# Kernel optimization log

Measured on AMD Instinct MI355X. Metric: run time of the kernel, lower is better.

Reference implementation:

```python
import jax, jax.numpy as jnp
import numpy as np

DIM = 768
H = 12
HD = 64  # head_dim = dim // num_heads
SCALE = HD ** (-0.5)
EPS = 1e-6


def setup_inputs() -> dict:
    key = jax.random.key(0)
    k1, k2, k3, k4, k5 = jax.random.split(key, 5)
    B, N = 8, 1024
    x = jax.random.normal(k1, (B, N, DIM), dtype=jnp.float32)
    policy = jax.random.uniform(k2, (B, N, 1), dtype=jnp.float32)
    # nn.Linear weights: [out_features, in_features]; qkv_bias=False, proj has bias
    qkv_w = jax.random.normal(k3, (3 * H * HD, DIM), dtype=jnp.float32) * (DIM ** -0.5)
    proj_w = jax.random.normal(k4, (DIM, H * HD), dtype=jnp.float32) * ((H * HD) ** -0.5)
    proj_b = jax.random.normal(k5, (DIM,), dtype=jnp.float32) * 0.01
    return {"x": x, "policy": policy, "qkv_w": qkv_w, "proj_w": proj_w, "proj_b": proj_b}


def _softmax_with_policy(attn, policy):
    # attn: [B,H,N,N], policy: [B,N,1]
    B, Hh, N, _ = attn.shape
    attn_policy = policy.reshape(B, 1, 1, N)
    eye = jnp.eye(N, dtype=attn_policy.dtype).reshape(1, 1, N, N)
    attn_policy = attn_policy + (1.0 - attn_policy) * eye
    max_att = jnp.max(attn, axis=-1, keepdims=True)
    a = jnp.exp((attn - max_att).astype(jnp.float32)) * attn_policy.astype(jnp.float32)
    a = (a + EPS / N) / (jnp.sum(a, axis=-1, keepdims=True) + EPS)
    return a.astype(max_att.dtype)


def reference(x, policy, qkv_w, proj_w, proj_b):
    B, N, C = x.shape
    qkv = (x @ qkv_w.T).reshape(B, N, 3, H, HD)
    qkv = jnp.transpose(qkv, (2, 0, 3, 1, 4))  # [3,B,H,N,HD]
    q, k, v = qkv[0], qkv[1], qkv[2]
    attn = jnp.einsum('bhnd,bhmd->bhnm', q * SCALE, k)  # [B,H,N,N]
    attn = _softmax_with_policy(attn, policy)
    out = jnp.einsum('bhnm,bhmd->bhnd', attn, v)  # [B,H,N,HD]
    out = jnp.transpose(out, (0, 2, 1, 3)).reshape(B, N, H * HD)
    return out @ proj_w.T + proj_b
```

## Files before the change

kernel.cpp:

```cpp
#include <hip/hip_runtime.h>

typedef __bf16 bf16x8 __attribute__((ext_vector_type(8)));
typedef float floatx4 __attribute__((ext_vector_type(4)));

#define EPSF 1e-6f

__device__ inline unsigned short f2bf(float f) {
  union { float f; unsigned u; } x; x.f = f;
  unsigned r = x.u + 0x7FFFu + ((x.u >> 16) & 1u);
  return (unsigned short)(r >> 16);
}
__device__ inline float bf2f(unsigned short u) {
  union { unsigned u; float f; } x; x.u = ((unsigned)u) << 16;
  return x.f;
}
__device__ inline unsigned pk2bf(float lo, float hi) {
  union { float f; unsigned u; } a, b; a.f = lo; b.f = hi;
  unsigned ua = a.u + 0x8000u, ub = b.u + 0x8000u;
  return (ub & 0xFFFF0000u) | (ua >> 16);
}
__device__ inline unsigned cvtpk(float lo, float hi) {
  unsigned r;
  asm("v_cvt_pk_bf16_f32 %0, %1, %2" : "=v"(r) : "v"(lo), "v"(hi));
  return r;
}
__device__ inline float fexp2(float x) { return __builtin_amdgcn_exp2f(x); }

__device__ inline floatx4 mfma16(bf16x8 a, bf16x8 b, floatx4 c) {
  return __builtin_amdgcn_mfma_f32_16x16x32_bf16(a, b, c, 0, 0, 0);
}

__device__ inline void gll16(const unsigned short* g, unsigned short* l) {
  __builtin_amdgcn_global_load_lds((__attribute__((address_space(1))) void*)g,
                                   (__attribute__((address_space(3))) void*)l, 16, 0, 0);
}

__device__ __host__ inline int sigma_inv(int p) {
  const int qq = p >> 3, jj = p & 7;
  return (jj < 4) ? (qq * 4 + jj) : (16 + qq * 4 + jj - 4);
}

__global__ __launch_bounds__(256) void prep_kernel(const float* __restrict__ x,
                                                   const float* __restrict__ qkv_w,
                                                   const float* __restrict__ proj_w,
                                                   const float* __restrict__ policy,
                                                   unsigned short* __restrict__ xb,
                                                   unsigned short* __restrict__ wqkv,
                                                   unsigned short* __restrict__ wproj,
                                                   unsigned short* __restrict__ pbf) {
  const int bid = blockIdx.x, tid = threadIdx.x;
  if (bid < 3072) {
    const int i = bid * 2048 + tid * 8;
    float4 v0 = *(const float4*)(x + i);
    float4 v1 = *(const float4*)(x + i + 4);
    __align__(16) unsigned short o[8] = {f2bf(v0.x), f2bf(v0.y), f2bf(v0.z), f2bf(v0.w),
                                         f2bf(v1.x), f2bf(v1.y), f2bf(v1.z), f2bf(v1.w)};
    *(float4*)(xb + i) = *(float4*)o;
  } else if (bid < 3936) {
    const int i = (bid - 3072) * 2048 + tid * 8;
    const float s = (i < 589824) ? 0.18033688011112042f : 1.0f;
    float4 v0 = *(const float4*)(qkv_w + i);
    float4 v1 = *(const float4*)(qkv_w + i + 4);
    __align__(16) unsigned short o[8] = {
        f2bf(v0.x * s), f2bf(v0.y * s), f2bf(v0.z * s), f2bf(v0.w * s),
        f2bf(v1.x * s), f2bf(v1.y * s), f2bf(v1.z * s), f2bf(v1.w * s)};
    *(float4*)(wqkv + i) = *(float4*)o;
  } else if (bid < 4224) {
    const int i0 = (bid - 3936) * 2048 + tid * 8;
    const int base = (i0 / 768) * 768 + ((i0 % 768) & ~63);
    __align__(16) unsigned short o[8];
#pragma unroll
    for (int t = 0; t < 8; t++) {
      const int cp = (i0 + t) & 63;
      const int c = 16 * (cp & 3) + (cp >> 2);
      o[t] = f2bf(proj_w[base + c]);
    }
    *(float4*)(wproj + i0) = *(float4*)o;
  } else {
    const int idx = (bid - 4224) * 256 + tid;
    const int b = idx >> 10, g = idx & 1023;
    const int c = ((g >> 5) << 5) + sigma_inv(g & 31);
    pbf[idx] = f2bf(policy[b * 1024 + c]);
  }
}

template <int EP, int BN, int W>
__global__ __launch_bounds__(256, W) void gemm_bt(const unsigned short* __restrict__ A,
                                                  const unsigned short* __restrict__ Bt,
                                                  void* __restrict__ Cout,
                                                  const float* __restrict__ bias,
                                                  int M, int N, int K) {
  constexpr int J = BN / 32;
  __shared__ __align__(16) unsigned short sA[128 * 64];
  __shared__ __align__(16) unsigned short sB[BN * 64];
  const int bid = blockIdx.x;
  const int yb = (bid & 7) * 8 + ((bid >> 3) & 7);
  const int xb_ = bid >> 6;
  const int m0 = yb * 128, n0 = xb_ * BN;
  const int tid = threadIdx.x;
  const int lane = tid & 63, wave = tid >> 6;
  const int qd = lane >> 4, l15 = lane & 15;
  const int wr = (wave >> 1) * 64, wc = (wave & 1) * (BN / 2);
  const int srow = tid >> 3;
  const int scb = (tid & 7) ^ (srow & 7);
  const unsigned short* Ag = A + (long)(m0 + srow) * K + scb * 8;
  const unsigned short* Bg = Bt + (long)(n0 + srow) * K + scb * 8;
  const int x7 = l15 & 7;
  floatx4 acc[4][J] = {};
  for (int k0 = 0; k0 < K; k0 += 64) {
    __syncthreads();
#pragma unroll
    for (int p = 0; p < 4; p++) gll16(Ag + (long)(p * 32) * K + k0, sA + p * 2048 + wave * 512);
#pragma unroll
    for (int p = 0; p < J; p++) gll16(Bg + (long)(p * 32) * K + k0, sB + p * 2048 + wave * 512);
    __syncthreads();
#pragma unroll
    for (int s = 0; s < 2; s++) {
      const int cw = ((s * 4 + qd) ^ x7) * 8;
      bf16x8 af[4], bf[J];
#pragma unroll
      for (int i = 0; i < 4; i++) af[i] = *(const bf16x8*)&sA[(wr + i * 16 + l15) * 64 + cw];
#pragma unroll
      for (int j = 0; j < J; j++) bf[j] = *(const bf16x8*)&sB[(wc + j * 16 + l15) * 64 + cw];
#pragma unroll
      for (int i = 0; i < 4; i++)
#pragma unroll
        for (int j = 0; j < J; j++) acc[i][j] = mfma16(af[i], bf[j], acc[i][j]);
    }
  }
  if constexpr (EP == 0) {
#pragma unroll
    for (int i = 0; i < 4; i++)
#pragma unroll
      for (int r = 0; r < 4; r++) {
        const int row = m0 + wr + i * 16 + qd * 4 + r;
        __align__(8) unsigned short pk[4];
#pragma unroll
        for (int j = 0; j < 4; j++) pk[j] = f2bf(acc[i][j][r]);
        *(uint2*)((unsigned short*)Cout + (long)row * N + n0 + wc + 4 * l15) = *(uint2*)pk;
      }
  } else {
#pragma unroll
    for (int i = 0; i < 4; i++)
#pragma unroll
      for (int j = 0; j < J; j++) {
        const int col = n0 + wc + j * 16 + l15;
#pragma unroll
        for (int r = 0; r < 4; r++) {
          const int row = m0 + wr + i * 16 + qd * 4 + r;
          ((float*)Cout)[(long)row * N + col] = acc[i][j][r] + bias[col];
        }
      }
  }
}

__global__ __launch_bounds__(256) void transpose_v(const unsigned short* __restrict__ qkv,
                                                   const float* __restrict__ policy,
                                                   unsigned short* __restrict__ vTp) {
  __shared__ unsigned short tile[64][72];
  __shared__ float sPol[64];
  const int bh = blockIdx.y;
  const int b = bh / 12, h = bh % 12;
  const int n0 = blockIdx.x * 64;
  const int t = threadIdx.x;
  if (t < 64) sPol[t] = policy[b * 1024 + n0 + t];
  {
    const int nr = t >> 2, dc = (t & 3) * 16;
    const unsigned short* src = qkv + (long)(b * 1024 + n0 + nr) * 2304 + 2 * 768 + h * 64 + dc;
    float4 v0 = *(const float4*)src;
    float4 v1 = *(const float4*)(src + 8);
    *(float4*)&tile[nr][dc] = v0;
    *(float4*)&tile[nr][dc + 8] = v1;
  }
  __syncthreads();
  {
    const int d = t >> 2, nc = (t & 3) * 16;
    __align__(16) unsigned short o[16];
#pragma unroll
    for (int jj = 0; jj < 16; jj++) {
      const int cc = nc + jj;
      const int cl = (cc & 32) + sigma_inv(cc & 31);
      o[jj] = f2bf(bf2f(tile[cl][d]) * sPol[cl]);
    }
    unsigned short* dst = vTp + (long)(bh * 64 + d) * 1024 + n0 + nc;
    *(float4*)dst = *(float4*)&o[0];
    *(float4*)(dst + 8) = *(float4*)&o[8];
  }
}

__global__ __launch_bounds__(256, 3) void attn_kernel(const unsigned short* __restrict__ qkv,
                                                      const unsigned short* __restrict__ vTp,
                                                      const unsigned short* __restrict__ pbf,
                                                      const float* __restrict__ policy,
                                                      unsigned short* __restrict__ aout) {
  __shared__ __align__(16) unsigned short sK[4][2048];
  __shared__ __align__(16) unsigned short sV[4][2048];
  __shared__ __align__(16) unsigned short sPv[1024];
  __shared__ float sD[4][32];
  const int bid = blockIdx.x;
  const int bh = bid % 96, qt = bid / 96;
  const int b = bh / 12, h = bh % 12;
  const int tid = threadIdx.x;
  const int wave = tid >> 6, lane = tid & 63;
  const int qd = lane >> 4, l15 = lane & 15;
  const int q0 = qt * 128 + wave * 32;
  const unsigned short* qb = qkv + (long)(b * 1024 + q0 + l15) * 2304 + h * 64 + qd * 8;
  bf16x8 qf00 = *(const bf16x8*)qb;
  bf16x8 qf01 = *(const bf16x8*)(qb + 32);
  bf16x8 qf10 = *(const bf16x8*)(qb + (long)16 * 2304);
  bf16x8 qf11 = *(const bf16x8*)(qb + (long)16 * 2304 + 32);
  if (tid < 128) *(float4*)(sPv + tid * 8) = *(const float4*)(pbf + b * 1024 + tid * 8);
  const int krow = wave * 8 + (lane >> 3);
  const int kcb = (lane & 7) ^ (lane >> 3);
  const unsigned short* kgl = qkv + (long)(b * 1024 + krow) * 2304 + 768 + h * 64 + kcb * 8;
  const int vrow = tid >> 2;
  const int vcb = (tid & 3) ^ ((vrow ^ (vrow >> 2)) & 3);
  const unsigned short* vgl = vTp + (long)(bh * 64 + vrow) * 1024 + vcb * 8;
  const int x7 = l15 & 7;
  const int vsw = (qd ^ ((l15 ^ (l15 >> 2)) & 3)) * 8;
  floatx4 O0[4] = {}, O1[4] = {};
  floatx4 Dl0 = {}, Dl1 = {};
  const floatx4 z = {0.f, 0.f, 0.f, 0.f};
#pragma unroll
  for (int c = 0; c < 3; ++c) {
    gll16(kgl + (long)(32 * c) * 2304, &sK[c][wave * 512]);
    gll16(vgl + 32 * c, &sV[c][wave * 512]);
  }
  asm volatile("s_waitcnt vmcnt(2) lgkmcnt(0)" ::: "memory");
  __builtin_amdgcn_s_barrier();
  asm volatile("" ::: "memory");
  bf16x8 kA00 = *(const bf16x8*)&sK[0][(0 + l15) * 64 + ((0 + qd) ^ x7) * 8];
  bf16x8 kA01 = *(const bf16x8*)&sK[0][(0 + l15) * 64 + ((4 + qd) ^ x7) * 8];
  bf16x8 kA10 = *(const bf16x8*)&sK[0][(16 + l15) * 64 + ((0 + qd) ^ x7) * 8];
  bf16x8 kA11 = *(const bf16x8*)&sK[0][(16 + l15) * 64 + ((4 + qd) ^ x7) * 8];
  bf16x8 kB00, kB01, kB10, kB11;
  auto body = [&](int it, bf16x8& c00, bf16x8& c01, bf16x8& c10, bf16x8& c11,
                  bf16x8& n00, bf16x8& n01, bf16x8& n10, bf16x8& n11) {
    const int buf = it & 3;
    if (it < 29) {
      const long co = (long)(32 * (it + 3));
      gll16(kgl + co * 2304, &sK[(it + 3) & 3][wave * 512]);
      gll16(vgl + co, &sV[(it + 3) & 3][wave * 512]);
    }
    const int c0 = it * 32;
    bf16x8 pv = *(const bf16x8*)&sPv[c0 + qd * 8];
    __builtin_amdgcn_s_setprio(1);
    floatx4 tA0 = mfma16(c01, qf01, mfma16(c00, qf00, z));
    floatx4 tB0 = mfma16(c11, qf01, mfma16(c10, qf00, z));
    floatx4 tA1 = mfma16(c01, qf11, mfma16(c00, qf10, z));
    floatx4 tB1 = mfma16(c11, qf11, mfma16(c10, qf10, z));
    __builtin_amdgcn_s_setprio(0);
    const int nb = (it + 1) & 3;
    n00 = *(const bf16x8*)&sK[nb][(0 + l15) * 64 + ((0 + qd) ^ x7) * 8];
    n01 = *(const bf16x8*)&sK[nb][(0 + l15) * 64 + ((4 + qd) ^ x7) * 8];
    n10 = *(const bf16x8*)&sK[nb][(16 + l15) * 64 + ((0 + qd) ^ x7) * 8];
    n11 = *(const bf16x8*)&sK[nb][(16 + l15) * 64 + ((4 + qd) ^ x7) * 8];
    uint4 pu0, pu1;
    pu0.x = cvtpk(fexp2(tA0[0]), fexp2(tA0[1]));
    pu0.y = cvtpk(fexp2(tA0[2]), fexp2(tA0[3]));
    pu0.z = cvtpk(fexp2(tB0[0]), fexp2(tB0[1]));
    pu0.w = cvtpk(fexp2(tB0[2]), fexp2(tB0[3]));
    pu1.x = cvtpk(fexp2(tA1[0]), fexp2(tA1[1]));
    pu1.y = cvtpk(fexp2(tA1[2]), fexp2(tA1[3]));
    pu1.z = cvtpk(fexp2(tB1[0]), fexp2(tB1[1]));
    pu1.w = cvtpk(fexp2(tB1[2]), fexp2(tB1[3]));
    bf16x8 pf0 = *(bf16x8*)&pu0;
    bf16x8 pf1 = *(bf16x8*)&pu1;
    bf16x8 vf0 = *(const bf16x8*)&sV[buf][(0 * 16 + l15) * 32 + vsw];
    bf16x8 vf1 = *(const bf16x8*)&sV[buf][(1 * 16 + l15) * 32 + vsw];
    bf16x8 vf2 = *(const bf16x8*)&sV[buf][(2 * 16 + l15) * 32 + vsw];
    bf16x8 vf3 = *(const bf16x8*)&sV[buf][(3 * 16 + l15) * 32 + vsw];
    __builtin_amdgcn_s_setprio(1);
    Dl0 = mfma16(pf0, pv, Dl0);
    Dl1 = mfma16(pf1, pv, Dl1);
    O0[0] = mfma16(pf0, vf0, O0[0]); O1[0] = mfma16(pf1, vf0, O1[0]);
    O0[1] = mfma16(pf0, vf1, O0[1]); O1[1] = mfma16(pf1, vf1, O1[1]);
    O0[2] = mfma16(pf0, vf2, O0[2]); O1[2] = mfma16(pf1, vf2, O1[2]);
    O0[3] = mfma16(pf0, vf3, O0[3]); O1[3] = mfma16(pf1, vf3, O1[3]);
    __builtin_amdgcn_s_setprio(0);
    if (it < 29) asm volatile("s_waitcnt vmcnt(2)" ::: "memory");
    else         asm volatile("s_waitcnt vmcnt(0)" ::: "memory");
    __builtin_amdgcn_s_barrier();
    asm volatile("" ::: "memory");
  };
#pragma unroll 1
  for (int itp = 0; itp < 16; ++itp) {
    body(2 * itp,     kA00, kA01, kA10, kA11, kB00, kB01, kB10, kB11);
    body(2 * itp + 1, kB00, kB01, kB10, kB11, kA00, kA01, kA10, kA11);
  }
  {
    const unsigned short* kd = qkv + (long)(b * 1024 + q0 + l15) * 2304 + 768 + h * 64 + qd * 8;
    bf16x8 kd00 = *(const bf16x8*)kd;
    bf16x8 kd01 = *(const bf16x8*)(kd + 32);
    bf16x8 kd10 = *(const bf16x8*)(kd + (long)16 * 2304);
    bf16x8 kd11 = *(const bf16x8*)(kd + (long)16 * 2304 + 32);
    float part0 = 0.f, part1 = 0.f;
#pragma unroll
    for (int jj = 0; jj < 8; jj++) {
      part0 += (float)qf00[jj] * (float)kd00[jj] + (float)qf01[jj] * (float)kd01[jj];
      part1 += (float)qf10[jj] * (float)kd10[jj] + (float)qf11[jj] * (float)kd11[jj];
    }
    part0 += __shfl_xor(part0, 16); part0 += __shfl_xor(part0, 32);
    part1 += __shfl_xor(part1, 16); part1 += __shfl_xor(part1, 32);
    const float p0 = policy[b * 1024 + q0 + l15];
    const float p1 = policy[b * 1024 + q0 + 16 + l15];
    if (qd == 0) {
      sD[wave][l15] = fexp2(part0) * (1.0f - p0);
      sD[wave][16 + l15] = fexp2(part1) * (1.0f - p1);
    }
    __builtin_amdgcn_s_waitcnt(0);
    const unsigned short* vdiag = qkv + (long)(b * 1024 + q0) * 2304 + 1536 + h * 64 + l15;
#pragma unroll
    for (int r = 0; r < 4; r++) {
      const int row = qd * 4 + r;
      const float c0v = sD[wave][row], c1v = sD[wave][16 + row];
#pragma unroll
      for (int j = 0; j < 4; j++) {
        O0[j][r] += c0v * bf2f(vdiag[(long)row * 2304 + j * 16]);
        O1[j][r] += c1v * bf2f(vdiag[(long)(16 + row) * 2304 + j * 16]);
      }
      Dl0[r] += c0v;
      Dl1[r] += c1v;
    }
  }
  const long ob = (long)(b * 1024 + q0 + qd * 4) * 768 + h * 64 + l15;
#pragma unroll
  for (int r = 0; r < 4; r++) {
    const float li0 = 1.0f / (Dl0[r] + EPSF);
    const float li1 = 1.0f / (Dl1[r] + EPSF);
#pragma unroll
    for (int j = 0; j < 4; j++) {
      aout[ob + (long)r * 768 + j * 16] = f2bf(O0[j][r] * li0);
      aout[ob + (long)(16 * 768) + r * 768 + j * 16] = f2bf(O1[j][r] * li1);
    }
  }
}

extern "C" void kernel_launch(void* const* d_in, const int* in_sizes, int n_in,
                              void* d_out, int out_size, void* d_ws, size_t ws_size,
                              hipStream_t stream) {
  const float* x      = (const float*)d_in[0];
  const float* policy = (const float*)d_in[1];
  const float* qkv_w  = (const float*)d_in[2];
  const float* proj_w = (const float*)d_in[3];
  const float* proj_b = (const float*)d_in[4];
  float* out = (float*)d_out;

  char* ws = (char*)d_ws;
  unsigned short* xb    = (unsigned short*)(ws + 0);
  unsigned short* wqkv  = (unsigned short*)(ws + 12582912);
  unsigned short* wproj = (unsigned short*)(ws + 16121856);
  unsigned short* qkvb  = (unsigned short*)(ws + 17301504);
  unsigned short* vTp   = (unsigned short*)(ws + 55050240);
  unsigned short* aoutb = (unsigned short*)(ws + 67633152);
  unsigned short* pbf   = (unsigned short*)(ws + 80216064);

  prep_kernel<<<4256, 256, 0, stream>>>(x, qkv_w, proj_w, policy, xb, wqkv, wproj, pbf);
  gemm_bt<0, 128, 4><<<dim3(18 * 64), 256, 0, stream>>>(xb, wqkv, qkvb, nullptr, 8192, 2304, 768);
  transpose_v<<<dim3(16, 96), 256, 0, stream>>>(qkvb, policy, vTp);
  attn_kernel<<<dim3(768), 256, 0, stream>>>(qkvb, vTp, pbf, policy, aoutb);
  gemm_bt<1, 64, 3><<<dim3(12 * 64), 256, 0, stream>>>(aoutb, wproj, out, proj_b, 8192, 768, 768);
}
```

Measured before the change: 177.5 us.

## Process two K/V chunks per barrier with pairwise double-buffered prefetch

Restructures the attention inner loop so that each iteration handles two 32-key chunks, prefetching the next pair into the alternate half of the 4-slot LDS ring. This halves the number of workgroup barriers and vmcnt waits per key sweep. In exchange it uses a full vmcnt(0) wait before each barrier instead of a rolling depth-3 prefetch, so there is less slack for global-load latency. It also hoists the swizzled K offsets.

```diff
diff --git a/kernel.cpp b/kernel.cpp
--- a/kernel.cpp
+++ b/kernel.cpp
@@ -218,43 +218,29 @@
   const unsigned short* vgl = vTp + (long)(bh * 64 + vrow) * 1024 + vcb * 8;
   const int x7 = l15 & 7;
   const int vsw = (qd ^ ((l15 ^ (l15 >> 2)) & 3)) * 8;
+  const int ko0 = ((0 + qd) ^ x7) * 8, ko1 = ((4 + qd) ^ x7) * 8;
   floatx4 O0[4] = {}, O1[4] = {};
   floatx4 Dl0 = {}, Dl1 = {};
   const floatx4 z = {0.f, 0.f, 0.f, 0.f};
-#pragma unroll
-  for (int c = 0; c < 3; ++c) {
-    gll16(kgl + (long)(32 * c) * 2304, &sK[c][wave * 512]);
-    gll16(vgl + 32 * c, &sV[c][wave * 512]);
-  }
-  asm volatile("s_waitcnt vmcnt(2) lgkmcnt(0)" ::: "memory");
+  gll16(kgl, &sK[0][wave * 512]);
+  gll16(vgl, &sV[0][wave * 512]);
+  gll16(kgl + (long)32 * 2304, &sK[1][wave * 512]);
+  gll16(vgl + 32, &sV[1][wave * 512]);
+  asm volatile("s_waitcnt vmcnt(0) lgkmcnt(0)" ::: "memory");
   __builtin_amdgcn_s_barrier();
   asm volatile("" ::: "memory");
-  bf16x8 kA00 = *(const bf16x8*)&sK[0][(0 + l15) * 64 + ((0 + qd) ^ x7) * 8];
-  bf16x8 kA01 = *(const bf16x8*)&sK[0][(0 + l15) * 64 + ((4 + qd) ^ x7) * 8];
-  bf16x8 kA10 = *(const bf16x8*)&sK[0][(16 + l15) * 64 + ((0 + qd) ^ x7) * 8];
-  bf16x8 kA11 = *(const bf16x8*)&sK[0][(16 + l15) * 64 + ((4 + qd) ^ x7) * 8];
-  bf16x8 kB00, kB01, kB10, kB11;
-  auto body = [&](int it, bf16x8& c00, bf16x8& c01, bf16x8& c10, bf16x8& c11,
-                  bf16x8& n00, bf16x8& n01, bf16x8& n10, bf16x8& n11) {
-    const int buf = it & 3;
-    if (it < 29) {
-      const long co = (long)(32 * (it + 3));
-      gll16(kgl + co * 2304, &sK[(it + 3) & 3][wave * 512]);
-      gll16(vgl + co, &sV[(it + 3) & 3][wave * 512]);
-    }
-    const int c0 = it * 32;
+  bf16x8 kA00 = *(const bf16x8*)&sK[0][(0 + l15) * 64 + ko0];
+  bf16x8 kA01 = *(const bf16x8*)&sK[0][(0 + l15) * 64 + ko1];
+  bf16x8 kA10 = *(const bf16x8*)&sK[0][(16 + l15) * 64 + ko0];
+  bf16x8 kA11 = *(const bf16x8*)&sK[0][(16 + l15) * 64 + ko1];
+  auto chunk = [&](int c0, int vb, bf16x8 k00, bf16x8 k01, bf16x8 k10, bf16x8 k11) {
     bf16x8 pv = *(const bf16x8*)&sPv[c0 + qd * 8];
     __builtin_amdgcn_s_setprio(1);
-    floatx4 tA0 = mfma16(c01, qf01, mfma16(c00, qf00, z));
-    floatx4 tB0 = mfma16(c11, qf01, mfma16(c10, qf00, z));
-    floatx4 tA1 = mfma16(c01, qf11, mfma16(c00, qf10, z));
-    floatx4 tB1 = mfma16(c11, qf11, mfma16(c10, qf10, z));
+    floatx4 tA0 = mfma16(k01, qf01, mfma16(k00, qf00, z));
+    floatx4 tB0 = mfma16(k11, qf01, mfma16(k10, qf00, z));
+    floatx4 tA1 = mfma16(k01, qf11, mfma16(k00, qf10, z));
+    floatx4 tB1 = mfma16(k11, qf11, mfma16(k10, qf10, z));
     __builtin_amdgcn_s_setprio(0);
-    const int nb = (it + 1) & 3;
-    n00 = *(const bf16x8*)&sK[nb][(0 + l15) * 64 + ((0 + qd) ^ x7) * 8];
-    n01 = *(const bf16x8*)&sK[nb][(0 + l15) * 64 + ((4 + qd) ^ x7) * 8];
-    n10 = *(const bf16x8*)&sK[nb][(16 + l15) * 64 + ((0 + qd) ^ x7) * 8];
-    n11 = *(const bf16x8*)&sK[nb][(16 + l15) * 64 + ((4 + qd) ^ x7) * 8];
     uint4 pu0, pu1;
     pu0.x = cvtpk(fexp2(tA0[0]), fexp2(tA0[1]));
     pu0.y = cvtpk(fexp2(tA0[2]), fexp2(tA0[3]));
@@ -266,10 +252,10 @@
     pu1.w = cvtpk(fexp2(tB1[2]), fexp2(tB1[3]));
     bf16x8 pf0 = *(bf16x8*)&pu0;
     bf16x8 pf1 = *(bf16x8*)&pu1;
-    bf16x8 vf0 = *(const bf16x8*)&sV[buf][(0 * 16 + l15) * 32 + vsw];
-    bf16x8 vf1 = *(const bf16x8*)&sV[buf][(1 * 16 + l15) * 32 + vsw];
-    bf16x8 vf2 = *(const bf16x8*)&sV[buf][(2 * 16 + l15) * 32 + vsw];
-    bf16x8 vf3 = *(const bf16x8*)&sV[buf][(3 * 16 + l15) * 32 + vsw];
+    bf16x8 vf0 = *(const bf16x8*)&sV[vb][(0 * 16 + l15) * 32 + vsw];
+    bf16x8 vf1 = *(const bf16x8*)&sV[vb][(1 * 16 + l15) * 32 + vsw];
+    bf16x8 vf2 = *(const bf16x8*)&sV[vb][(2 * 16 + l15) * 32 + vsw];
+    bf16x8 vf3 = *(const bf16x8*)&sV[vb][(3 * 16 + l15) * 32 + vsw];
     __builtin_amdgcn_s_setprio(1);
     Dl0 = mfma16(pf0, pv, Dl0);
     Dl1 = mfma16(pf1, pv, Dl1);
@@ -278,15 +264,33 @@
     O0[2] = mfma16(pf0, vf2, O0[2]); O1[2] = mfma16(pf1, vf2, O1[2]);
     O0[3] = mfma16(pf0, vf3, O0[3]); O1[3] = mfma16(pf1, vf3, O1[3]);
     __builtin_amdgcn_s_setprio(0);
-    if (it < 29) asm volatile("s_waitcnt vmcnt(2)" ::: "memory");
-    else         asm volatile("s_waitcnt vmcnt(0)" ::: "memory");
+  };
+#pragma unroll 1
+  for (int s = 0; s < 16; ++s) {
+    const int cb0 = (s & 1) ? 2 : 0;
+    const int cb1 = cb0 + 1;
+    if (s < 15) {
+      const long co = (long)(64 * s + 64);
+      gll16(kgl + co * 2304, &sK[cb0 ^ 2][wave * 512]);
+      gll16(vgl + co, &sV[cb0 ^ 2][wave * 512]);
+      gll16(kgl + (co + 32) * 2304, &sK[cb1 ^ 2][wave * 512]);
+      gll16(vgl + co + 32, &sV[cb1 ^ 2][wave * 512]);
+    }
+    bf16x8 kB00 = *(const bf16x8*)&sK[cb1][(0 + l15) * 64 + ko0];
+    bf16x8 kB01 = *(const bf16x8*)&sK[cb1][(0 + l15) * 64 + ko1];
+    bf16x8 kB10 = *(const bf16x8*)&sK[cb1][(16 + l15) * 64 + ko0];
+    bf16x8 kB11 = *(const bf16x8*)&sK[cb1][(16 + l15) * 64 + ko1];
+    chunk(64 * s, cb0, kA00, kA01, kA10, kA11);
+    chunk(64 * s + 32, cb1, kB00, kB01, kB10, kB11);
+    asm volatile("s_waitcnt vmcnt(0)" ::: "memory");
     __builtin_amdgcn_s_barrier();
     asm volatile("" ::: "memory");
-  };
-#pragma unroll 1
-  for (int itp = 0; itp < 16; ++itp) {
-    body(2 * itp,     kA00, kA01, kA10, kA11, kB00, kB01, kB10, kB11);
-    body(2 * itp + 1, kB00, kB01, kB10, kB11, kA00, kA01, kA10, kA11);
+    if (s < 15) {
+      kA00 = *(const bf16x8*)&sK[cb0 ^ 2][(0 + l15) * 64 + ko0];
+      kA01 = *(const bf16x8*)&sK[cb0 ^ 2][(0 + l15) * 64 + ko1];
+      kA10 = *(const bf16x8*)&sK[cb0 ^ 2][(16 + l15) * 64 + ko0];
+      kA11 = *(const bf16x8*)&sK[cb0 ^ 2][(16 + l15) * 64 + ko1];
+    }
   }
   {
     const unsigned short* kd = qkv + (long)(b * 1024 + q0 + l15) * 2304 + 768 + h * 64 + qd * 8;
```

New measurement: 175.7 us (median of 2 runs). About the same (-1.0%).
